# Optimization experiments

Measured on AMD Instinct MI355X. Metric: run time of the kernel, lower is better.

## Reference

```python
import math
import jax, jax.numpy as jnp
import numpy as np

B, T, D, H = 2, 2048, 1024, 16
HD = D // H  # 64


def _rope(x, freq_cis):
    # x: (B, T, H, HD); freq_cis: (1, T, 1, HD//2) complex
    Bx, Tx, Hx, Dx = x.shape
    xc = jax.lax.complex(x[..., 0::2], x[..., 1::2])
    xr = xc * freq_cis
    return jnp.stack([xr.real, xr.imag], axis=-1).reshape(Bx, Tx, Hx, Dx)


def setup_inputs() -> dict:
    key = jax.random.key(0)
    ks = jax.random.split(key, 10)
    x = jax.random.normal(ks[0], (B, T, D), dtype=jnp.float32)
    # causal mask, broadcast over batch and heads
    mask = jnp.tril(jnp.ones((T, T), dtype=bool))[None, None]
    # RoPE angles: theta_j = 10000^{-2j/HD}, angle[t, j] = t * theta_j
    inv_freq = 1.0 / (10000.0 ** (jnp.arange(0, HD, 2, dtype=jnp.float32) / HD))  # (HD/2,)
    freqs = (jnp.arange(T, dtype=jnp.float32)[:, None] * inv_freq[None, :])[None, :, None, :]  # (1,T,1,HD/2)
    s = 1.0 / math.sqrt(D)
    Wq = jax.random.normal(ks[1], (D, D), dtype=jnp.float32) * s
    bq = jnp.zeros((D,), dtype=jnp.float32)
    Wk = jax.random.normal(ks[2], (D, D), dtype=jnp.float32) * s
    bk = jnp.zeros((D,), dtype=jnp.float32)
    Wv = jax.random.normal(ks[3], (D, D), dtype=jnp.float32) * s
    bv = jnp.zeros((D,), dtype=jnp.float32)
    Wo = jax.random.normal(ks[4], (D, D), dtype=jnp.float32) * s
    bo = jnp.zeros((D,), dtype=jnp.float32)
    return {"x": x, "mask": mask, "freqs": freqs,
            "Wq": Wq, "bq": bq, "Wk": Wk, "bk": bk,
            "Wv": Wv, "bv": bv, "Wo": Wo, "bo": bo}


def reference(x, mask, freqs, Wq, bq, Wk, bk, Wv, bv, Wo, bo):
    Bx, Tx, Dx = x.shape
    freq_cis = jax.lax.complex(jnp.cos(freqs), jnp.sin(freqs))  # (1,T,1,HD/2)
    q = (x @ Wq + bq).reshape(Bx, Tx, H, HD)
    k = (x @ Wk + bk).reshape(Bx, Tx, H, HD)
    v = (x @ Wv + bv).reshape(Bx, Tx, H, HD)
    q = _rope(q, freq_cis)
    k = _rope(k, freq_cis)
    # (B, H, T, HD)
    q = q.transpose(0, 2, 1, 3)
    k = k.transpose(0, 2, 1, 3)
    v = v.transpose(0, 2, 1, 3)
    attn = jnp.einsum('bhqd,bhkd->bhqk', q, k) / math.sqrt(HD)
    attn = jnp.where(mask, attn, -1e9)
    probs = jax.nn.softmax(attn, axis=-1)  # dropout is identity (deterministic=True)
    out = jnp.einsum('bhqk,bhkd->bhqd', probs, v)
    out = out.transpose(0, 2, 1, 3).reshape(Bx, Tx, Dx)
    return out @ Wo + bo
```

## Files before the change

### kernel.cpp

```cpp
#include <hip/hip_runtime.h>
#include <cstdint>
#include <cstddef>

typedef __bf16 bf16x8 __attribute__((ext_vector_type(8)));
typedef float  f32x4  __attribute__((ext_vector_type(4)));

#define DEV __device__ __forceinline__

DEV unsigned short f2bf(float f) {
  union { float f; unsigned u; } x; x.f = f;
  unsigned r = x.u + 0x7fffu + ((x.u >> 16) & 1u);
  return (unsigned short)(r >> 16);
}

DEV float fexp2(float x) {
  float r;
  asm("v_exp_f32 %0, %1" : "=v"(r) : "v"(x));
  return r;
}

DEV void gl_lds16(const void* g, void* l) {
  __builtin_amdgcn_global_load_lds((const __attribute__((address_space(1))) void*)g,
                                   (__attribute__((address_space(3))) void*)l, 16, 0, 0);
}

DEV bf16x8 lds_frag(const void* base, int byteoff) {
  return *reinterpret_cast<const bf16x8*>(reinterpret_cast<const char*>(base) + byteoff);
}

DEV f32x4 MFMA(bf16x8 a, bf16x8 b, f32x4 c) {
  return __builtin_amdgcn_mfma_f32_16x16x32_bf16(a, b, c, 0, 0, 0);
}

#define KL2E 0.18033688011112042f

__global__ __launch_bounds__(256) void k_cast_x(const float* __restrict__ x,
                                                unsigned short* __restrict__ xb) {
  int i = (blockIdx.x * 256 + threadIdx.x) * 8;
  float4 a = *(const float4*)(x + i);
  float4 b = *(const float4*)(x + i + 4);
  uint4 o;
  o.x = (unsigned)f2bf(a.x) | ((unsigned)f2bf(a.y) << 16);
  o.y = (unsigned)f2bf(a.z) | ((unsigned)f2bf(a.w) << 16);
  o.z = (unsigned)f2bf(b.x) | ((unsigned)f2bf(b.y) << 16);
  o.w = (unsigned)f2bf(b.z) | ((unsigned)f2bf(b.w) << 16);
  *reinterpret_cast<uint4*>(xb + i) = o;
}

__global__ __launch_bounds__(256) void k_trans_w(const float* __restrict__ Wq, const float* __restrict__ Wk,
                                                 const float* __restrict__ Wv, const float* __restrict__ Wo,
                                                 unsigned short* __restrict__ WT) {
  __shared__ float tile[32][33];
  int z = blockIdx.z;
  const float* W = (z == 0) ? Wq : ((z == 1) ? Wk : ((z == 2) ? Wv : Wo));
  float scl = (z == 0) ? KL2E : 1.0f;
  unsigned short* out = WT + ((size_t)z << 20);
  int x = threadIdx.x, y = threadIdx.y;
  int gx = blockIdx.x * 32 + x;
  int gy = blockIdx.y * 32;
#pragma unroll
  for (int i = 0; i < 4; ++i) tile[y + i * 8][x] = W[(size_t)(gy + y + i * 8) * 1024 + gx];
  __syncthreads();
#pragma unroll
  for (int i = 0; i < 4; ++i)
    out[(size_t)(blockIdx.x * 32 + y + i * 8) * 1024 + gy + x] = f2bf(tile[x][y + i * 8] * scl);
}

__global__ __launch_bounds__(256) void k_cs(const float* __restrict__ freqs, float* __restrict__ tab) {
  int i = blockIdx.x * 256 + threadIdx.x;
  float a = freqs[i];
  float s, c;
  sincosf(a, &s, &c);
  ((float2*)tab)[i] = make_float2(c, s);
}

__global__ __launch_bounds__(256) void k_qkv(const unsigned short* __restrict__ xb,
                                             const unsigned short* __restrict__ WT,
                                             const float* __restrict__ bq,
                                             const float* __restrict__ bk,
                                             const float* __restrict__ bv,
                                             const float* __restrict__ tab,
                                             unsigned short* __restrict__ qws,
                                             unsigned short* __restrict__ kws,
                                             unsigned short* __restrict__ vws) {
  __shared__ __align__(16) unsigned short As[2][128 * 32];
  __shared__ __align__(16) unsigned short Bs[2][128 * 32];
  int t = threadIdx.x, w = t >> 6, l = t & 63;
  int z = blockIdx.z;
  int n0 = blockIdx.x * 128, m0 = blockIdx.y * 128;
  const unsigned short* Wz = WT + ((size_t)z << 20);
  int wm = w >> 1, wn = w & 1;
  f32x4 zero4 = {0.f, 0.f, 0.f, 0.f};
  f32x4 acc[4][4];
#pragma unroll
  for (int i = 0; i < 4; ++i)
#pragma unroll
    for (int j = 0; j < 4; ++j) acc[i][j] = zero4;

  int aoff[4], boff[4];
#pragma unroll
  for (int i = 0; i < 4; ++i) {
    aoff[i] = ((wm * 64 + i * 16 + (l & 15)) * 32 + ((l >> 4) * 8)) * 2;
    boff[i] = ((wn * 64 + i * 16 + (l & 15)) * 32 + ((l >> 4) * 8)) * 2;
  }
  int r0 = t >> 2, c0 = t & 3;

#define QSTAGE(k0v, buf) do { \
    char* la = (char*)As + (buf) * 8192 + w * 1024; \
    char* lb = (char*)Bs + (buf) * 8192 + w * 1024; \
    const char* ga0 = (const char*)xb + ((size_t)(m0 + r0) * 1024 + (k0v) + c0 * 8) * 2; \
    const char* ga1 = (const char*)xb + ((size_t)(m0 + 64 + r0) * 1024 + (k0v) + c0 * 8) * 2; \
    const char* gb0 = (const char*)Wz + ((size_t)(n0 + r0) * 1024 + (k0v) + c0 * 8) * 2; \
    const char* gb1 = (const char*)Wz + ((size_t)(n0 + 64 + r0) * 1024 + (k0v) + c0 * 8) * 2; \
    gl_lds16(ga0, la); gl_lds16(ga1, la + 4096); \
    gl_lds16(gb0, lb); gl_lds16(gb1, lb + 4096); \
  } while (0)

  QSTAGE(0, 0);
  asm volatile("s_waitcnt vmcnt(0)" ::: "memory");
  __syncthreads();
  for (int k0 = 0; k0 < 1024; k0 += 32) {
    int cur = (k0 >> 5) & 1;
    if (k0 + 32 < 1024) QSTAGE(k0 + 32, cur ^ 1);
    const char* Ab = (const char*)As + cur * 8192;
    const char* Bb = (const char*)Bs + cur * 8192;
    bf16x8 af[4], bfr[4];
#pragma unroll
    for (int i = 0; i < 4; ++i) af[i] = lds_frag(Ab, aoff[i]);
#pragma unroll
    for (int i = 0; i < 4; ++i) bfr[i] = lds_frag(Bb, boff[i]);
#pragma unroll
    for (int i = 0; i < 4; ++i)
#pragma unroll
      for (int jn = 0; jn < 4; ++jn) acc[i][jn] = MFMA(af[i], bfr[jn], acc[i][jn]);
    asm volatile("s_waitcnt vmcnt(0)" ::: "memory");
    __syncthreads();
  }
#undef QSTAGE

  const float* bias = (z == 0) ? bq : ((z == 1) ? bk : bv);
  unsigned short* outp = (z == 0) ? qws : ((z == 1) ? kws : vws);
  float bscl = (z == 0) ? KL2E : 1.0f;
  bool doRope = (z < 2);
  int nb = n0 + wn * 64, mb = m0 + wm * 64;
#pragma unroll
  for (int i = 0; i < 4; ++i) {
#pragma unroll
    for (int jn = 0; jn < 4; ++jn) {
      int n = nb + jn * 16 + (l & 15);
      float bsv = bias[n] * bscl;
      int hd = n & 63;
#pragma unroll
      for (int j = 0; j < 4; ++j) {
        int m = mb + i * 16 + ((l >> 4) << 2) + j;
        float val = acc[i][jn][j] + bsv;
        if (doRope) {
          int trow = m & 2047;
          float2 cs = ((const float2*)tab)[trow * 32 + (hd >> 1)];
          float part = __shfl_xor(val, 1);
          val = (hd & 1) ? fmaf(part, cs.y, val * cs.x) : fmaf(val, cs.x, -part * cs.y);
        }
        ((__bf16*)outp)[(size_t)m * 1024 + n] = (__bf16)val;
      }
    }
  }
}

__global__ __launch_bounds__(256) void k_vtrans(const unsigned short* __restrict__ vb,
                                                unsigned short* __restrict__ vtb) {
  __shared__ unsigned short vt[64 * 72];
  int t = threadIdx.x;
  int tt = blockIdx.x, bh = blockIdx.y;
  int b = bh >> 4, h = bh & 15;
  int row = t >> 2, ch = t & 3;
  const char* src = (const char*)vb + (((size_t)(b * 2048 + tt * 64 + row) * 1024) + h * 64 + ch * 16) * 2;
  uint4 v0 = *(const uint4*)src;
  uint4 v1 = *(const uint4*)(src + 16);
  const unsigned short* e0 = (const unsigned short*)&v0;
  const unsigned short* e1 = (const unsigned short*)&v1;
#pragma unroll
  for (int i = 0; i < 8; ++i) vt[(ch * 16 + i) * 72 + row] = e0[i];
#pragma unroll
  for (int i = 0; i < 8; ++i) vt[(ch * 16 + 8 + i) * 72 + row] = e1[i];
  __syncthreads();
  int hd = t >> 2, c2 = t & 3;
  uint4 o0 = *(const uint4*)&vt[hd * 72 + c2 * 16];
  uint4 o1 = *(const uint4*)&vt[hd * 72 + c2 * 16 + 8];
  char* dst = (char*)vtb + (((size_t)(bh * 64 + hd) * 2048) + tt * 64 + c2 * 16) * 2;
  *(uint4*)dst = o0;
  *(uint4*)(dst + 16) = o1;
}

DEV void attn_strip(const bf16x8 (&qf)[2], const bf16x8 (&kc)[2][4], const bf16x8 (&vc)[2][4],
                    f32x4 (&po)[4], f32x4 &lsum, float (&m_run)[4],
                    bool diag, unsigned short* pw, int w, int l) {
  int hi = l >> 4, lo = l & 15;
  f32x4 minit = {-m_run[0], -m_run[1], -m_run[2], -m_run[3]};
  f32x4 ps[4];
#pragma unroll
  for (int bn = 0; bn < 4; ++bn) ps[bn] = minit;
  __builtin_amdgcn_s_setprio(1);
#pragma unroll
  for (int ks = 0; ks < 2; ++ks)
#pragma unroll
    for (int bn = 0; bn < 4; ++bn) ps[bn] = MFMA(qf[ks], kc[ks][bn], ps[bn]);
  __builtin_amdgcn_s_setprio(0);
  if (diag) {
#pragma unroll
    for (int bn = 0; bn < 4; ++bn) {
      int kv = bn * 16 + lo;
#pragma unroll
      for (int j = 0; j < 4; ++j) {
        int r = (hi << 2) + j;
        if (kv > w * 16 + r) ps[bn][j] = -1e30f;
      }
    }
  }
  float t0 = fmaxf(fmaxf(ps[0][0], ps[0][1]), fmaxf(ps[0][2], ps[0][3]));
  float t1 = fmaxf(fmaxf(ps[1][0], ps[1][1]), fmaxf(ps[1][2], ps[1][3]));
  float t2 = fmaxf(fmaxf(ps[2][0], ps[2][1]), fmaxf(ps[2][2], ps[2][3]));
  float t3 = fmaxf(fmaxf(ps[3][0], ps[3][1]), fmaxf(ps[3][2], ps[3][3]));
  float tm = fmaxf(fmaxf(t0, t1), fmaxf(t2, t3));
  if (__any(tm > 8.0f)) {
    float rm[4];
#pragma unroll
    for (int j = 0; j < 4; ++j)
      rm[j] = fmaxf(fmaxf(ps[0][j], ps[1][j]), fmaxf(ps[2][j], ps[3][j]));
#pragma unroll
    for (int off = 1; off < 16; off <<= 1)
#pragma unroll
      for (int j = 0; j < 4; ++j) rm[j] = fmaxf(rm[j], __shfl_xor(rm[j], off));
    float d[4], al[4];
#pragma unroll
    for (int j = 0; j < 4; ++j) {
      d[j] = fmaxf(rm[j], 0.f);
      al[j] = fexp2(-d[j]);
      m_run[j] += d[j];
    }
#pragma unroll
    for (int bn = 0; bn < 4; ++bn)
#pragma unroll
      for (int j = 0; j < 4; ++j) ps[bn][j] -= d[j];
#pragma unroll
    for (int hf = 0; hf < 4; ++hf)
#pragma unroll
      for (int j = 0; j < 4; ++j) po[hf][j] *= al[j];
#pragma unroll
    for (int j = 0; j < 4; ++j) lsum[j] *= al[j];
  }
#pragma unroll
  for (int bn = 0; bn < 4; ++bn)
#pragma unroll
    for (int j = 0; j < 4; ++j) {
      int r = (hi << 2) + j, c = bn * 16 + lo;
      ((__bf16*)pw)[r * 64 + (((c >> 3) ^ (r & 7)) << 3) + (c & 7)] = (__bf16)fexp2(ps[bn][j]);
    }
  asm volatile("" ::: "memory");
  __bf16 one = (__bf16)1.0f;
  bf16x8 ones = {one, one, one, one, one, one, one, one};
  __builtin_amdgcn_s_setprio(1);
#pragma unroll
  for (int ks = 0; ks < 2; ++ks) {
    bf16x8 pa = lds_frag(pw, lo * 128 + (((ks * 4 + hi) ^ (lo & 7)) << 4));
#pragma unroll
    for (int hf = 0; hf < 4; ++hf) po[hf] = MFMA(pa, vc[ks][hf], po[hf]);
    lsum = MFMA(pa, ones, lsum);
  }
  __builtin_amdgcn_s_setprio(0);
  asm volatile("" ::: "memory");
}

__global__ __launch_bounds__(256) void k_attn(const unsigned short* __restrict__ qb,
                                              const unsigned short* __restrict__ kb,
                                              const unsigned short* __restrict__ vtb,
                                              unsigned short* __restrict__ ab) {
  __shared__ __align__(16) unsigned short Ks[2][64 * 64];
  __shared__ __align__(16) unsigned short Vts[2][64 * 64];
  __shared__ __align__(16) unsigned short PsA[4 * 16 * 64];
  __shared__ __align__(16) unsigned short PsB[4 * 16 * 64];
  int t = threadIdx.x, w = t >> 6, l = t & 63;
  int lid = blockIdx.x;
  int xcd = lid & 7, rest = lid >> 3;
  int bh = xcd + 8 * (rest & 3);
  int pi = rest >> 2;
  int qtA = pi, qtB = 31 - pi;
  int b = bh >> 4, h = bh & 15;
  int hi = l >> 4, lo = l & 15;

  bf16x8 qfA[2], qfB[2];
  {
    int mA = b * 2048 + qtA * 64 + w * 16 + lo;
    const char* qp = (const char*)qb + ((size_t)mA * 1024 + h * 64 + hi * 8) * 2;
    qfA[0] = *(const bf16x8*)qp;
    qfA[1] = *(const bf16x8*)(qp + 64);
    int mB = b * 2048 + qtB * 64 + w * 16 + lo;
    const char* qp2 = (const char*)qb + ((size_t)mB * 1024 + h * 64 + hi * 8) * 2;
    qfB[0] = *(const bf16x8*)qp2;
    qfB[1] = *(const bf16x8*)(qp2 + 64);
  }
  f32x4 zero4 = {0.f, 0.f, 0.f, 0.f};
  f32x4 poA[4], poB[4], lsumA = zero4, lsumB = zero4;
  float mA_[4], mB_[4];
#pragma unroll
  for (int i = 0; i < 4; ++i) {
    poA[i] = zero4; poB[i] = zero4;
    mA_[i] = 0.f;  mB_[i] = 0.f;
  }
  unsigned short* pwA = PsA + w * 1024;
  unsigned short* pwB = PsB + w * 1024;
  int r0 = t >> 3, s0 = t & 7, lc0 = s0 ^ (r0 & 7);
  int r1 = 32 + r0;
  const char* kbase = (const char*)kb + ((size_t)(b * 2048) * 1024 + h * 64) * 2;
  const char* vbase = (const char*)vtb + ((size_t)bh * 64) * 2048 * 2;

#define ASTAGE(jt, buf) do { \
    char* lk = (char*)Ks + (buf) * 8192 + w * 1024; \
    char* lv = (char*)Vts + (buf) * 8192 + w * 1024; \
    const char* gk0 = kbase + ((size_t)((jt) * 64 + r0) * 1024) * 2 + lc0 * 16; \
    const char* gk1 = kbase + ((size_t)((jt) * 64 + r1) * 1024) * 2 + lc0 * 16; \
    const char* gv0 = vbase + (size_t)r0 * 4096 + (jt) * 128 + lc0 * 16; \
    const char* gv1 = vbase + (size_t)r1 * 4096 + (jt) * 128 + lc0 * 16; \
    gl_lds16(gk0, lk); gl_lds16(gk1, lk + 4096); \
    gl_lds16(gv0, lv); gl_lds16(gv1, lv + 4096); \
  } while (0)

  ASTAGE(0, 0);
  asm volatile("s_waitcnt vmcnt(0)" ::: "memory");
  __syncthreads();
  for (int jt = 0; jt <= qtB; ++jt) {
    int cur = jt & 1;
    if (jt < qtB) ASTAGE(jt + 1, cur ^ 1);
    const char* Kb = (const char*)Ks + cur * 8192;
    const char* Vb = (const char*)Vts + cur * 8192;
    bf16x8 kc[2][4], vc[2][4];
#pragma unroll
    for (int ks = 0; ks < 2; ++ks)
#pragma unroll
      for (int i = 0; i < 4; ++i) {
        int row = i * 16 + lo;
        kc[ks][i] = lds_frag(Kb, row * 128 + (((ks * 4 + hi) ^ (lo & 7)) << 4));
        vc[ks][i] = lds_frag(Vb, row * 128 + (((ks * 4 + hi) ^ (lo & 7)) << 4));
      }
    attn_strip(qfB, kc, vc, poB, lsumB, mB_, jt == qtB, pwB, w, l);
    if (jt <= qtA) attn_strip(qfA, kc, vc, poA, lsumA, mA_, jt == qtA, pwA, w, l);
    asm volatile("s_waitcnt vmcnt(0)" ::: "memory");
    __syncthreads();
  }
#undef ASTAGE

#pragma unroll
  for (int s = 0; s < 2; ++s) {
    f32x4* po = s ? poB : poA;
    f32x4 ls = s ? lsumB : lsumA;
    int qt = s ? qtB : qtA;
    float inv[4];
#pragma unroll
    for (int j = 0; j < 4; ++j) inv[j] = 1.0f / ls[j];
#pragma unroll
    for (int hf = 0; hf < 4; ++hf)
#pragma unroll
      for (int j = 0; j < 4; ++j) {
        int r = (hi << 2) + j;
        int m = b * 2048 + qt * 64 + w * 16 + r;
        int col = h * 64 + hf * 16 + lo;
        ((__bf16*)ab)[(size_t)m * 1024 + col] = (__bf16)(po[hf][j] * inv[j]);
      }
  }
}

__global__ __launch_bounds__(256) void k_oproj(const unsigned short* __restrict__ ab,
                                               const unsigned short* __restrict__ WoT,
                                               const float* __restrict__ bo,
                                               float* __restrict__ out) {
  __shared__ __align__(16) unsigned short As[2][128 * 32];
  __shared__ __align__(16) unsigned short Bs[2][128 * 32];
  int t = threadIdx.x, w = t >> 6, l = t & 63;
  int n0 = blockIdx.x * 128, m0 = blockIdx.y * 128;
  int wm = w >> 1, wn = w & 1;
  f32x4 zero4 = {0.f, 0.f, 0.f, 0.f};
  f32x4 acc[4][4];
#pragma unroll
  for (int i = 0; i < 4; ++i)
#pragma unroll
    for (int j = 0; j < 4; ++j) acc[i][j] = zero4;
  int aoff[4], boff[4];
#pragma unroll
  for (int i = 0; i < 4; ++i) {
    aoff[i] = ((wm * 64 + i * 16 + (l & 15)) * 32 + ((l >> 4) * 8)) * 2;
    boff[i] = ((wn * 64 + i * 16 + (l & 15)) * 32 + ((l >> 4) * 8)) * 2;
  }
  int r0 = t >> 2, c0 = t & 3;

#define OSTAGE(k0v, buf) do { \
    char* la = (char*)As + (buf) * 8192 + w * 1024; \
    char* lb = (char*)Bs + (buf) * 8192 + w * 1024; \
    const char* ga0 = (const char*)ab + ((size_t)(m0 + r0) * 1024 + (k0v) + c0 * 8) * 2; \
    const char* ga1 = (const char*)ab + ((size_t)(m0 + 64 + r0) * 1024 + (k0v) + c0 * 8) * 2; \
    const char* gb0 = (const char*)WoT + ((size_t)(n0 + r0) * 1024 + (k0v) + c0 * 8) * 2; \
    const char* gb1 = (const char*)WoT + ((size_t)(n0 + 64 + r0) * 1024 + (k0v) + c0 * 8) * 2; \
    gl_lds16(ga0, la); gl_lds16(ga1, la + 4096); \
    gl_lds16(gb0, lb); gl_lds16(gb1, lb + 4096); \
  } while (0)

  OSTAGE(0, 0);
  asm volatile("s_waitcnt vmcnt(0)" ::: "memory");
  __syncthreads();
  for (int k0 = 0; k0 < 1024; k0 += 32) {
    int cur = (k0 >> 5) & 1;
    if (k0 + 32 < 1024) OSTAGE(k0 + 32, cur ^ 1);
    const char* Ab = (const char*)As + cur * 8192;
    const char* Bb = (const char*)Bs + cur * 8192;
    bf16x8 af[4], bfr[4];
#pragma unroll
    for (int i = 0; i < 4; ++i) af[i] = lds_frag(Ab, aoff[i]);
#pragma unroll
    for (int i = 0; i < 4; ++i) bfr[i] = lds_frag(Bb, boff[i]);
#pragma unroll
    for (int i = 0; i < 4; ++i)
#pragma unroll
      for (int jn = 0; jn < 4; ++jn) acc[i][jn] = MFMA(af[i], bfr[jn], acc[i][jn]);
    asm volatile("s_waitcnt vmcnt(0)" ::: "memory");
    __syncthreads();
  }
#undef OSTAGE

  int nb = n0 + wn * 64, mb = m0 + wm * 64;
#pragma unroll
  for (int i = 0; i < 4; ++i)
#pragma unroll
    for (int jn = 0; jn < 4; ++jn) {
      int n = nb + jn * 16 + (l & 15);
      float bsv = bo[n];
#pragma unroll
      for (int j = 0; j < 4; ++j) {
        int m = mb + i * 16 + ((l >> 4) << 2) + j;
        out[(size_t)m * 1024 + n] = acc[i][jn][j] + bsv;
      }
    }
}

extern "C" void kernel_launch(void* const* d_in, const int* in_sizes, int n_in,
                              void* d_out, int out_size, void* d_ws, size_t ws_size,
                              hipStream_t stream) {
  const float* x     = (const float*)d_in[0];
  const float* freqs = (const float*)d_in[2];
  const float* Wq    = (const float*)d_in[3];
  const float* bq    = (const float*)d_in[4];
  const float* Wk    = (const float*)d_in[5];
  const float* bk    = (const float*)d_in[6];
  const float* Wv    = (const float*)d_in[7];
  const float* bv    = (const float*)d_in[8];
  const float* Wo    = (const float*)d_in[9];
  const float* bo    = (const float*)d_in[10];

  char* ws = (char*)d_ws;
  unsigned short* xb  = (unsigned short*)(ws);
  unsigned short* WT  = (unsigned short*)(ws + ((size_t)8 << 20));
  unsigned short* qb  = (unsigned short*)(ws + ((size_t)16 << 20));
  unsigned short* kb  = (unsigned short*)(ws + ((size_t)24 << 20));
  unsigned short* vb  = (unsigned short*)(ws + ((size_t)32 << 20));
  unsigned short* vtb = (unsigned short*)(ws + ((size_t)40 << 20));
  unsigned short* ab  = (unsigned short*)(ws + ((size_t)48 << 20));
  float*          tab = (float*)(ws + ((size_t)56 << 20));

  k_cast_x<<<2048, 256, 0, stream>>>(x, xb);
  k_trans_w<<<dim3(32, 32, 4), dim3(32, 8), 0, stream>>>(Wq, Wk, Wv, Wo, WT);
  k_cs<<<256, 256, 0, stream>>>(freqs, tab);
  k_qkv<<<dim3(8, 32, 3), 256, 0, stream>>>(xb, WT, bq, bk, bv, tab, qb, kb, vb);
  k_vtrans<<<dim3(32, 32), 256, 0, stream>>>(vb, vtb);
  k_attn<<<dim3(512), 256, 0, stream>>>(qb, kb, vtb, ab);
  k_oproj<<<dim3(8, 32), 256, 0, stream>>>(ab, WT + ((size_t)3 << 20), bo, (float*)d_out);
}
```

Measured before the change: 246.7 us.

## Overlap next-stage global loads with compute and halve oproj M tile

In the QKV, attention and output-projection loops, the kernel now waits only for the current stage's loads (partial vmcnt) before a barrier, so the prefetch of the next stage stays in flight during the MFMA work instead of being drained at the end of each iteration. Raw s_barrier replaces __syncthreads. The output projection tile shrinks from 128x128 to 64x128, doubling the grid to 512 blocks to fill more CUs. The cost is less reuse per block in oproj and reliance on vmcnt ordering being correct with LDS-direct loads.

```diff
diff --git a/kernel.cpp b/kernel.cpp
--- a/kernel.cpp
+++ b/kernel.cpp
@@ -33,6 +33,7 @@
 }
 
 #define KL2E 0.18033688011112042f
+#define BARRIER __builtin_amdgcn_s_barrier()
 
 __global__ __launch_bounds__(256) void k_cast_x(const float* __restrict__ x,
                                                 unsigned short* __restrict__ xb) {
@@ -118,10 +119,16 @@
 
   QSTAGE(0, 0);
   asm volatile("s_waitcnt vmcnt(0)" ::: "memory");
-  __syncthreads();
+  BARRIER;
   for (int k0 = 0; k0 < 1024; k0 += 32) {
     int cur = (k0 >> 5) & 1;
-    if (k0 + 32 < 1024) QSTAGE(k0 + 32, cur ^ 1);
+    if (k0 + 32 < 1024) {
+      QSTAGE(k0 + 32, cur ^ 1);
+      asm volatile("s_waitcnt vmcnt(4)" ::: "memory");
+    } else {
+      asm volatile("s_waitcnt vmcnt(0)" ::: "memory");
+    }
+    BARRIER;
     const char* Ab = (const char*)As + cur * 8192;
     const char* Bb = (const char*)Bs + cur * 8192;
     bf16x8 af[4], bfr[4];
@@ -133,8 +140,7 @@
     for (int i = 0; i < 4; ++i)
 #pragma unroll
       for (int jn = 0; jn < 4; ++jn) acc[i][jn] = MFMA(af[i], bfr[jn], acc[i][jn]);
-    asm volatile("s_waitcnt vmcnt(0)" ::: "memory");
-    __syncthreads();
+    BARRIER;
   }
 #undef QSTAGE
 
@@ -326,10 +332,16 @@
 
   ASTAGE(0, 0);
   asm volatile("s_waitcnt vmcnt(0)" ::: "memory");
-  __syncthreads();
+  BARRIER;
   for (int jt = 0; jt <= qtB; ++jt) {
     int cur = jt & 1;
-    if (jt < qtB) ASTAGE(jt + 1, cur ^ 1);
+    if (jt < qtB) {
+      ASTAGE(jt + 1, cur ^ 1);
+      asm volatile("s_waitcnt vmcnt(4)" ::: "memory");
+    } else {
+      asm volatile("s_waitcnt vmcnt(0)" ::: "memory");
+    }
+    BARRIER;
     const char* Kb = (const char*)Ks + cur * 8192;
     const char* Vb = (const char*)Vts + cur * 8192;
     bf16x8 kc[2][4], vc[2][4];
@@ -343,8 +355,7 @@
       }
     attn_strip(qfB, kc, vc, poB, lsumB, mB_, jt == qtB, pwB, w, l);
     if (jt <= qtA) attn_strip(qfA, kc, vc, poA, lsumA, mA_, jt == qtA, pwA, w, l);
-    asm volatile("s_waitcnt vmcnt(0)" ::: "memory");
-    __syncthreads();
+    BARRIER;
   }
 #undef ASTAGE
 
@@ -372,61 +383,67 @@
                                                const unsigned short* __restrict__ WoT,
                                                const float* __restrict__ bo,
                                                float* __restrict__ out) {
-  __shared__ __align__(16) unsigned short As[2][128 * 32];
+  __shared__ __align__(16) unsigned short As[2][64 * 32];
   __shared__ __align__(16) unsigned short Bs[2][128 * 32];
   int t = threadIdx.x, w = t >> 6, l = t & 63;
-  int n0 = blockIdx.x * 128, m0 = blockIdx.y * 128;
+  int n0 = blockIdx.x * 128, m0 = blockIdx.y * 64;
   int wm = w >> 1, wn = w & 1;
   f32x4 zero4 = {0.f, 0.f, 0.f, 0.f};
-  f32x4 acc[4][4];
+  f32x4 acc[2][4];
+#pragma unroll
+  for (int i = 0; i < 2; ++i)
+#pragma unroll
+    for (int j = 0; j < 4; ++j) acc[i][j] = zero4;
+  int aoff[2], boff[4];
+#pragma unroll
+  for (int i = 0; i < 2; ++i)
+    aoff[i] = ((wm * 32 + i * 16 + (l & 15)) * 32 + ((l >> 4) * 8)) * 2;
 #pragma unroll
   for (int i = 0; i < 4; ++i)
-#pragma unroll
-    for (int j = 0; j < 4; ++j) acc[i][j] = zero4;
-  int aoff[4], boff[4];
-#pragma unroll
-  for (int i = 0; i < 4; ++i) {
-    aoff[i] = ((wm * 64 + i * 16 + (l & 15)) * 32 + ((l >> 4) * 8)) * 2;
     boff[i] = ((wn * 64 + i * 16 + (l & 15)) * 32 + ((l >> 4) * 8)) * 2;
-  }
-  int r0 = t >> 2, c0 = t & 3;
+  int ra = t >> 2, ca = t & 3;
 
 #define OSTAGE(k0v, buf) do { \
-    char* la = (char*)As + (buf) * 8192 + w * 1024; \
-    char* lb = (char*)Bs + (buf) * 8192 + w * 1024; \
-    const char* ga0 = (const char*)ab + ((size_t)(m0 + r0) * 1024 + (k0v) + c0 * 8) * 2; \
-    const char* ga1 = (const char*)ab + ((size_t)(m0 + 64 + r0) * 1024 + (k0v) + c0 * 8) * 2; \
-    const char* gb0 = (const char*)WoT + ((size_t)(n0 + r0) * 1024 + (k0v) + c0 * 8) * 2; \
-    const char* gb1 = (const char*)WoT + ((size_t)(n0 + 64 + r0) * 1024 + (k0v) + c0 * 8) * 2; \
-    gl_lds16(ga0, la); gl_lds16(ga1, la + 4096); \
-    gl_lds16(gb0, lb); gl_lds16(gb1, lb + 4096); \
+    char* la = (char*)As + (buf) * 4096; \
+    char* lb = (char*)Bs + (buf) * 8192; \
+    const char* ga = (const char*)ab + ((size_t)(m0 + ra) * 1024 + (k0v) + ca * 8) * 2; \
+    const char* gb0 = (const char*)WoT + ((size_t)(n0 + ra) * 1024 + (k0v) + ca * 8) * 2; \
+    const char* gb1 = (const char*)WoT + ((size_t)(n0 + 64 + ra) * 1024 + (k0v) + ca * 8) * 2; \
+    gl_lds16(ga, la + t * 16); \
+    gl_lds16(gb0, lb + t * 16); \
+    gl_lds16(gb1, lb + 4096 + t * 16); \
   } while (0)
 
   OSTAGE(0, 0);
   asm volatile("s_waitcnt vmcnt(0)" ::: "memory");
-  __syncthreads();
+  BARRIER;
   for (int k0 = 0; k0 < 1024; k0 += 32) {
     int cur = (k0 >> 5) & 1;
-    if (k0 + 32 < 1024) OSTAGE(k0 + 32, cur ^ 1);
-    const char* Ab = (const char*)As + cur * 8192;
+    if (k0 + 32 < 1024) {
+      OSTAGE(k0 + 32, cur ^ 1);
+      asm volatile("s_waitcnt vmcnt(3)" ::: "memory");
+    } else {
+      asm volatile("s_waitcnt vmcnt(0)" ::: "memory");
+    }
+    BARRIER;
+    const char* Ab = (const char*)As + cur * 4096;
     const char* Bb = (const char*)Bs + cur * 8192;
-    bf16x8 af[4], bfr[4];
-#pragma unroll
-    for (int i = 0; i < 4; ++i) af[i] = lds_frag(Ab, aoff[i]);
+    bf16x8 af[2], bfr[4];
+#pragma unroll
+    for (int i = 0; i < 2; ++i) af[i] = lds_frag(Ab, aoff[i]);
 #pragma unroll
     for (int i = 0; i < 4; ++i) bfr[i] = lds_frag(Bb, boff[i]);
 #pragma unroll
-    for (int i = 0; i < 4; ++i)
+    for (int i = 0; i < 2; ++i)
 #pragma unroll
       for (int jn = 0; jn < 4; ++jn) acc[i][jn] = MFMA(af[i], bfr[jn], acc[i][jn]);
-    asm volatile("s_waitcnt vmcnt(0)" ::: "memory");
-    __syncthreads();
+    BARRIER;
   }
 #undef OSTAGE
 
-  int nb = n0 + wn * 64, mb = m0 + wm * 64;
-#pragma unroll
-  for (int i = 0; i < 4; ++i)
+  int nb = n0 + wn * 64, mb = m0 + wm * 32;
+#pragma unroll
+  for (int i = 0; i < 2; ++i)
 #pragma unroll
     for (int jn = 0; jn < 4; ++jn) {
       int n = nb + jn * 16 + (l & 15);
@@ -469,5 +486,5 @@
   k_qkv<<<dim3(8, 32, 3), 256, 0, stream>>>(xb, WT, bq, bk, bv, tab, qb, kb, vb);
   k_vtrans<<<dim3(32, 32), 256, 0, stream>>>(vb, vtb);
   k_attn<<<dim3(512), 256, 0, stream>>>(qb, kb, vtb, ab);
-  k_oproj<<<dim3(8, 32), 256, 0, stream>>>(ab, WT + ((size_t)3 << 20), bo, (float*)d_out);
-}
+  k_oproj<<<dim3(8, 64), 256, 0, stream>>>(ab, WT + ((size_t)3 << 20), bo, (float*)d_out);
+}
```

After: 245.4 us. About the same (-0.5%).
